# Kernel tuning notes

Hardware: AMD Instinct MI355X
Metric: run time of the kernel (lower is better)

The kernel has to match this reference:

```python
import jax, jax.numpy as jnp
import numpy as np

B, F, S = 2, 512, 1024
E = 4
I = 1024          # intermediate = 2 * features
K = 3             # conv kernel size
INIT_SCALE = 1.0
EPS = 1e-5
SLOPE = 0.02


def setup_inputs() -> dict:
    key = jax.random.key(0)
    k = jax.random.split(key, 6)
    inp = jax.random.normal(k[0], (B, F, S), jnp.float32)
    divisor = (jnp.arange(S, dtype=jnp.float32) + 1.0).reshape(1, 1, S)
    w0_gate = jax.random.normal(k[1], (E, F, 1), jnp.float32) * (F ** -0.5)
    w0 = jax.random.normal(k[2], (E, F, 3 * I), jnp.float32) * (F ** -0.5)
    w1 = jax.random.normal(k[3], (3 * I, I, K), jnp.float32) * ((I * K) ** -0.5)
    w2_gate = jax.random.normal(k[4], (E, I, 1), jnp.float32) * (I ** -0.5)
    w2 = jax.random.normal(k[5], (E, I, F), jnp.float32) * (I ** -0.5)
    return {"inp": inp, "divisor": divisor, "w0_gate": w0_gate, "w0": w0,
            "w1": w1, "w2_gate": w2_gate, "w2": w2}


def _norm(x):
    # channel norm over dim 1: subtract mean, divide by scaled L2 norm
    x = x - jnp.mean(x, axis=1, keepdims=True)
    n = jnp.sqrt(jnp.sum(x * x, axis=1, keepdims=True)) * (x.shape[1] ** -0.5)
    return x / (n + EPS)


def _moe(x, gate, w):
    # x: [B,F,S]; gate: [E,F,1]; w: [E,F,D]
    logits = jnp.einsum('bfs,ef->bes', x, gate[:, :, 0])          # [B,E,S]
    gates = jax.nn.softmax(logits, axis=1)
    idx = jnp.argmax(logits, axis=1)                              # [B,S]
    one_hot = jax.nn.one_hot(idx, w.shape[0], dtype=x.dtype)      # [B,S,E]
    # straight-through gumbel-style gate: hard one-hot fwd, soft grad
    gumbel = jnp.transpose(one_hot, (0, 2, 1)) - jax.lax.stop_gradient(gates) + gates  # [B,E,S]
    xs = jnp.transpose(x, (0, 2, 1))                              # [B,S,F]
    out = jnp.zeros((x.shape[0], x.shape[2], w.shape[2]), x.dtype)
    for e in range(w.shape[0]):  # small fixed expert count
        mask = one_hot[:, :, e][:, :, None]                       # [B,S,1]
        out = out + mask * ((xs * gumbel[:, e, :, None]) @ w[e])
    loss = jnp.sum(jnp.mean(gates, axis=(0, 2)) * jnp.mean(one_hot, axis=(0, 1)))
    return loss, jnp.transpose(out, (0, 2, 1))                    # [B,D,S]


def _conv1d(x, w, causal_pad):
    if causal_pad and w.shape[-1] > 1:
        x = jnp.pad(x, ((0, 0), (0, 0), (w.shape[-1] - 1, 0)))
    return jax.lax.conv_general_dilated(
        x, w, window_strides=(1,), padding='VALID',
        dimension_numbers=('NCH', 'OIH', 'NCH'), feature_group_count=1)


def reference(inp, divisor, w0_gate, w0, w1, w2_gate, w2):
    loss0, h = _moe(inp, w0_gate, w0)                 # [B,3I,S]
    depth, scale, shift = jnp.split(h, 3, axis=1)     # each [B,I,S]
    cum = jnp.cumsum(depth, axis=-1)
    h = jax.nn.leaky_relu(_norm(cum / divisor * scale + shift), SLOPE)
    h = _conv1d(h, w1, causal_pad=True)               # [B,3I,S]
    s0, s1, sh = jnp.split(h, 3, axis=1)
    h = jax.nn.leaky_relu(_norm(s0 * s1 + sh), SLOPE)
    loss1, out = _moe(h, w2_gate, w2)                 # [B,F,S]
    return out * INIT_SCALE, loss0 + loss1
```

## Files before the change

### kernel.cpp

```cpp
#include <hip/hip_runtime.h>
#include <hip/hip_bf16.h>

#define SDIM 1024

typedef float f32x4 __attribute__((ext_vector_type(4)));
typedef short short8 __attribute__((ext_vector_type(8)));

__device__ __forceinline__ unsigned short f2bf(float f) {
    __hip_bfloat16 h = __float2bfloat16(f);
    return *reinterpret_cast<unsigned short*>(&h);
}
__device__ __forceinline__ float bf2f(unsigned short u) {
    return __uint_as_float(((unsigned int)u) << 16);
}
__device__ __forceinline__ void gload_lds16(const unsigned short* g, unsigned short* l) {
    __builtin_amdgcn_global_load_lds((const __attribute__((address_space(1))) void*)g,
                                     (__attribute__((address_space(3))) void*)l, 16, 0, 0);
}

__device__ __forceinline__ void tr_split(
    const float* __restrict__ in, unsigned short* __restrict__ oh,
    unsigned short* __restrict__ ol, int R, int C, size_t sliceStride,
    int bx, int by, int slice, int tid, float (*t)[33])
{
    int c0 = bx * 32, r0 = by * 32;
    int cc = tid & 31, r8 = tid >> 5;
    const float* ip = in + slice * sliceStride;
    #pragma unroll
    for (int k = 0; k < 4; ++k) {
        int r = r8 + k * 8;
        t[r][cc] = ip[(size_t)(r0 + r) * C + c0 + cc];
    }
    __syncthreads();
    #pragma unroll
    for (int k = 0; k < 4; ++k) {
        int rr = r8 + k * 8;
        float v = t[cc][rr];
        unsigned short hi = f2bf(v);
        unsigned short lo = f2bf(v - bf2f(hi));
        size_t o = slice * sliceStride + (size_t)(c0 + rr) * R + r0 + cc;
        oh[o] = hi; ol[o] = lo;
    }
}

__global__ __launch_bounds__(256) void prep_kernel(
    const float* __restrict__ inp, const float* __restrict__ w0,
    const float* __restrict__ w1,
    unsigned short* __restrict__ xTh, unsigned short* __restrict__ xTl,
    unsigned short* __restrict__ w0Th, unsigned short* __restrict__ w0Tl,
    unsigned short* __restrict__ w1Th, unsigned short* __restrict__ w1Tl,
    const float* __restrict__ wg, int* __restrict__ idx, float* __restrict__ acc)
{
    __shared__ float t[32][33];
    __shared__ float wgs[4 * 512];
    __shared__ float part[32][4][9];
    __shared__ float la[8];
    int id = blockIdx.x;
    int tid = threadIdx.x;
    if (id < 1024) {
        int bx = id & 31, by = (id >> 5) & 15, slice = id >> 9;
        tr_split(inp, xTh, xTl, 512, 1024, (size_t)512 * 1024, bx, by, slice, tid, t);
    } else if (id < 7168) {
        int m = id - 1024;
        int bx = m % 96, by = (m / 96) & 15, slice = m / 1536;
        tr_split(w0, w0Th, w0Tl, 512, 3072, (size_t)512 * 3072, bx, by, slice, tid, t);
    } else if (id < 19456) {
        int tt = (id - 7168) * 256 + tid;
        int o = tt >> 10, i = tt & 1023;
        const float* p = w1 + (size_t)o * 3072 + i * 3;
        #pragma unroll
        for (int k = 0; k < 3; ++k) {
            float v = p[k];
            unsigned short hi = f2bf(v);
            unsigned short lo = f2bf(v - bf2f(hi));
            size_t off = (size_t)k * 3145728 + (size_t)o * 1024 + i;
            w1Th[off] = hi; w1Tl[off] = lo;
        }
    } else {
        if (tid < 8) la[tid] = 0.f;
        for (int l = tid; l < 2048; l += 256) wgs[l] = wg[l];
        __syncthreads();
        int t0 = (id - 19456) * 8;
        int b = t0 >> 10, s0 = t0 & 1023;
        int sl = tid & 7, fg = tid >> 3;
        float l0 = 0.f, l1 = 0.f, l2 = 0.f, l3 = 0.f;
        for (int f = fg; f < 512; f += 32) {
            float xv = inp[((size_t)b * 512 + f) * SDIM + s0 + sl];
            l0 += xv * wgs[f];
            l1 += xv * wgs[512 + f];
            l2 += xv * wgs[1024 + f];
            l3 += xv * wgs[1536 + f];
        }
        part[fg][0][sl] = l0; part[fg][1][sl] = l1;
        part[fg][2][sl] = l2; part[fg][3][sl] = l3;
        __syncthreads();
        for (int h = 16; h >= 1; h >>= 1) {
            if (fg < h) {
                #pragma unroll
                for (int e = 0; e < 4; ++e) part[fg][e][sl] += part[fg + h][e][sl];
            }
            __syncthreads();
        }
        if (fg == 0) {
            float L[4] = {part[0][0][sl], part[0][1][sl], part[0][2][sl], part[0][3][sl]};
            float m = fmaxf(fmaxf(L[0], L[1]), fmaxf(L[2], L[3]));
            float e0 = expf(L[0] - m), e1 = expf(L[1] - m), e2 = expf(L[2] - m), e3 = expf(L[3] - m);
            float inv = 1.0f / (e0 + e1 + e2 + e3);
            int best = 0; float bv = L[0];
            if (L[1] > bv) { bv = L[1]; best = 1; }
            if (L[2] > bv) { bv = L[2]; best = 2; }
            if (L[3] > bv) { bv = L[3]; best = 3; }
            idx[t0 + sl] = best;
            atomicAdd(&la[0], e0 * inv);
            atomicAdd(&la[1], e1 * inv);
            atomicAdd(&la[2], e2 * inv);
            atomicAdd(&la[3], e3 * inv);
            atomicAdd(&la[4 + best], 1.0f);
        }
        __syncthreads();
        if (tid < 8) atomicAdd(&acc[tid], la[tid]);
    }
}

__global__ __launch_bounds__(1024) void sort_kernel(
    const int* __restrict__ idx, int* __restrict__ perm, int* __restrict__ eSorted)
{
    int b = blockIdx.x;
    int tid = threadIdx.x;
    int lane = tid & 63, w = tid >> 6;
    int e = idx[(b << 10) + tid];
    __shared__ int wcnt[16][4];
    __shared__ int woff[16][4];
    int r = 0;
    unsigned long long lt = (1ull << lane) - 1ull;
    #pragma unroll
    for (int eo = 0; eo < 4; ++eo) {
        unsigned long long m = __ballot(e == eo);
        if (lane == 0) wcnt[w][eo] = __popcll(m);
        if (e == eo) r = __popcll(m & lt);
    }
    __syncthreads();
    if (tid == 0) {
        int baseAcc = 0;
        for (int eo = 0; eo < 4; ++eo)
            for (int ww = 0; ww < 16; ++ww) { woff[ww][eo] = baseAcc; baseAcc += wcnt[ww][eo]; }
    }
    __syncthreads();
    int pos = woff[w][e] + r;
    perm[(b << 10) + pos] = tid;
    eSorted[(b << 10) + pos] = e;
}

__global__ __launch_bounds__(256) void moe_split_kernel(
    const unsigned short* __restrict__ base, unsigned int XH, unsigned int XL,
    unsigned int WH, unsigned int WL,
    const int* __restrict__ perm, const int* __restrict__ eSorted,
    float* __restrict__ out, int Fdim, int Ddim)
{
    __shared__ unsigned short lds[768 * 32];
    int id = blockIdx.x;
    int chunk = gridDim.x >> 3;
    int wg = (id & 7) * chunk + (id >> 3);
    int t0 = (wg & 15) * 128;
    int d0 = (wg >> 4) * 64;
    int b = t0 >> 10, s0 = t0 & 1023;
    int tid = threadIdx.x;
    int lane = tid & 63;
    int lm = lane & 15, q = lane >> 4;
    int wid = tid >> 6;
    int wm = (wid >> 1) * 32, wn = (wid & 1) * 64;

    int eLo = eSorted[(b << 10) + s0];
    int eHi = eSorted[(b << 10) + s0 + 127];

    unsigned int gofs[12];
    int lofs[12], doSeg[12];
    #pragma unroll
    for (int j = 0; j < 12; ++j) {
        int seg = wid + 4 * j;
        int row = seg * 16 + (lane >> 2);
        int slot = lane & 3;
        int c = slot ^ ((row >> 1) & 3);
        unsigned int src;
        int act = 1;
        if (row < 256) {
            int gr = (row < 128) ? row : row - 128;
            unsigned int hb = (row < 128) ? XH : XL;
            int tj = perm[(b << 10) + s0 + gr];
            src = hb + (unsigned int)(((b << 10) + tj) * Fdim) + c * 8;
        } else {
            int R = row - 256;
            unsigned int hb = WH;
            if (R >= 256) { R -= 256; hb = WL; }
            int e = R >> 6;
            act = (e >= eLo && e <= eHi) ? 1 : 0;
            src = hb + (unsigned int)((e * Ddim + d0 + (R & 63)) * Fdim) + c * 8;
        }
        gofs[j] = src; lofs[j] = seg * 512 + lane * 8; doSeg[j] = act;
    }

    int bofH[4];
    #pragma unroll
    for (int fn = 0; fn < 4; ++fn) {
        int rh = wn + fn * 16 + lm;
        bofH[fn] = rh * 32 + ((q ^ ((rh >> 1) & 3)) << 3);
    }
    int aofH[4][2], aofL[4][2];
    #pragma unroll
    for (int e = 0; e < 4; ++e)
        #pragma unroll
        for (int fm = 0; fm < 2; ++fm) {
            int rh = 256 + e * 64 + wm + fm * 16 + lm;
            int rl = rh + 256;
            aofH[e][fm] = rh * 32 + ((q ^ ((rh >> 1) & 3)) << 3);
            aofL[e][fm] = rl * 32 + ((q ^ ((rl >> 1) & 3)) << 3);
        }

    int eidx[4], sv[4];
    #pragma unroll
    for (int fn = 0; fn < 4; ++fn) {
        int sl = (b << 10) + s0 + wn + fn * 16 + lm;
        eidx[fn] = eSorted[sl];
        sv[fn]   = perm[sl];
    }
    bool presF[4][4], presE[4];
    #pragma unroll
    for (int e = 0; e < 4; ++e) {
        presE[e] = false;
        #pragma unroll
        for (int fn = 0; fn < 4; ++fn) {
            presF[e][fn] = __any(eidx[fn] == e);
            presE[e] = presE[e] || presF[e][fn];
        }
    }

    f32x4 acc[2][4];
    #pragma unroll
    for (int fm = 0; fm < 2; ++fm)
        #pragma unroll
        for (int fn = 0; fn < 4; ++fn)
            acc[fm][fn] = (f32x4){0.f, 0.f, 0.f, 0.f};

    const short8 z = {0, 0, 0, 0, 0, 0, 0, 0};

    for (int f0 = 0; f0 < Fdim; f0 += 32) {
        __syncthreads();
        #pragma unroll
        for (int j = 0; j < 12; ++j)
            if (doSeg[j]) gload_lds16(base + gofs[j] + f0, lds + lofs[j]);
        __syncthreads();

        short8 bh[4], bl[4];
        #pragma unroll
        for (int fn = 0; fn < 4; ++fn) {
            bh[fn] = *(const short8*)(lds + bofH[fn]);
            bl[fn] = *(const short8*)(lds + bofH[fn] + 4096);
        }
        #pragma unroll
        for (int e = 0; e < 4; ++e) {
            if (presE[e]) {
                short8 ah[2], al[2];
                #pragma unroll
                for (int fm = 0; fm < 2; ++fm) {
                    ah[fm] = *(const short8*)(lds + aofH[e][fm]);
                    al[fm] = *(const short8*)(lds + aofL[e][fm]);
                }
                #pragma unroll
                for (int fn = 0; fn < 4; ++fn) {
                    if (presF[e][fn]) {
                        short8 bmH = (eidx[fn] == e) ? bh[fn] : z;
                        short8 bmL = (eidx[fn] == e) ? bl[fn] : z;
                        #pragma unroll
                        for (int fm = 0; fm < 2; ++fm) {
                            acc[fm][fn] = __builtin_amdgcn_mfma_f32_16x16x32_bf16(ah[fm], bmH, acc[fm][fn], 0, 0, 0);
                            acc[fm][fn] = __builtin_amdgcn_mfma_f32_16x16x32_bf16(ah[fm], bmL, acc[fm][fn], 0, 0, 0);
                            acc[fm][fn] = __builtin_amdgcn_mfma_f32_16x16x32_bf16(al[fm], bmH, acc[fm][fn], 0, 0, 0);
                        }
                    }
                }
            }
        }
    }

    #pragma unroll
    for (int fm = 0; fm < 2; ++fm)
        #pragma unroll
        for (int fn = 0; fn < 4; ++fn) {
            int d = d0 + wm + fm * 16 + q * 4;
            float* op = out + ((size_t)b * Ddim + d) * SDIM + sv[fn];
            #pragma unroll
            for (int r = 0; r < 4; ++r)
                op[(size_t)r * SDIM] = acc[fm][fn][r];
        }
}

__global__ __launch_bounds__(768) void conv_split_kernel(
    const unsigned short* __restrict__ base, unsigned int GH, unsigned int GL,
    unsigned int WH, unsigned int WL, unsigned int ZB, float* __restrict__ co)
{
    extern __shared__ unsigned short lds[];
    const int BUF = 35328;
    int id = blockIdx.x;
    int wg = (id & 7) * 32 + (id >> 3);
    int t0 = (wg & 7) * 256;
    int o0 = (wg >> 3) * 96;
    int b = t0 >> 10, s0 = t0 & 1023;
    int tid = threadIdx.x;
    int lane = tid & 63;
    int lm = lane & 15, q = lane >> 4;
    int wid = tid >> 6;
    int wm = (wid >> 2) * 32, wn = (wid & 3) * 64;

    unsigned int gofs[6];
    int lofs[6];
    int nseg = (wid < 9) ? 6 : 5;
    #pragma unroll
    for (int j = 0; j < 6; ++j) {
        int seg = wid + 12 * j;
        gofs[j] = ZB; lofs[j] = 0;
        if (seg < 69) {
            int row = seg * 16 + (lane >> 2);
            int slot = lane & 3;
            int c = slot ^ ((row >> 1) & 3);
            unsigned int src;
            if (row < 528) {
                int gr = (row < 264) ? row : row - 264;
                unsigned int hb = (row < 264) ? GH : GL;
                int s = s0 - 2 + gr;
                if (s < 0) src = ZB + c * 8;
                else { if (s > 1023) s = 1023;
                       src = hb + ((unsigned int)((b << 10) + s) << 10) + c * 8; }
            } else {
                int R = row - 528;
                unsigned int hb = WH;
                if (R >= 288) { R -= 288; hb = WL; }
                int k = R / 96, ol = R - k * 96;
                src = hb + (unsigned int)k * 3145728u + ((unsigned int)(o0 + ol) << 10) + c * 8;
            }
            gofs[j] = src;
            lofs[j] = seg * 512 + lane * 8;
        }
    }

    int aofH[3][2], aofL[3][2], bofH[3][4], bofL[3][4];
    #pragma unroll
    for (int k = 0; k < 3; ++k) {
        #pragma unroll
        for (int fm = 0; fm < 2; ++fm) {
            int R = k * 96 + wm + fm * 16 + lm;
            int rh = 528 + R, rl = 816 + R;
            aofH[k][fm] = rh * 32 + ((q ^ ((rh >> 1) & 3)) << 3);
            aofL[k][fm] = rl * 32 + ((q ^ ((rl >> 1) & 3)) << 3);
        }
        #pragma unroll
        for (int fn = 0; fn < 4; ++fn) {
            int rh = wn + fn * 16 + lm + k;
            int rl = rh + 264;
            bofH[k][fn] = rh * 32 + ((q ^ ((rh >> 1) & 3)) << 3);
            bofL[k][fn] = rl * 32 + ((q ^ ((rl >> 1) & 3)) << 3);
        }
    }

    f32x4 acc[2][4];
    #pragma unroll
    for (int fm = 0; fm < 2; ++fm)
        #pragma unroll
        for (int fn = 0; fn < 4; ++fn)
            acc[fm][fn] = (f32x4){0.f, 0.f, 0.f, 0.f};

    #pragma unroll
    for (int j = 0; j < 6; ++j)
        if (j < nseg) gload_lds16(base + gofs[j], lds + lofs[j]);

    int curOfs = 0;
    for (int i0 = 0; i0 < 1024; i0 += 32) {
        __syncthreads();
        int nxtOfs = curOfs ^ BUF;
        if (i0 + 32 < 1024) {
            #pragma unroll
            for (int j = 0; j < 6; ++j)
                if (j < nseg) gload_lds16(base + gofs[j] + i0 + 32, lds + nxtOfs + lofs[j]);
        }

        const unsigned short* lb = lds + curOfs;
        #pragma unroll
        for (int k = 0; k < 3; ++k) {
            short8 ah[2], al[2], bh[4], bl[4];
            #pragma unroll
            for (int fm = 0; fm < 2; ++fm) {
                ah[fm] = *(const short8*)(lb + aofH[k][fm]);
                al[fm] = *(const short8*)(lb + aofL[k][fm]);
            }
            #pragma unroll
            for (int fn = 0; fn < 4; ++fn) {
                bh[fn] = *(const short8*)(lb + bofH[k][fn]);
                bl[fn] = *(const short8*)(lb + bofL[k][fn]);
            }
            __builtin_amdgcn_s_setprio(1);
            #pragma unroll
            for (int fm = 0; fm < 2; ++fm)
                #pragma unroll
                for (int fn = 0; fn < 4; ++fn) {
                    acc[fm][fn] = __builtin_amdgcn_mfma_f32_16x16x32_bf16(ah[fm], bh[fn], acc[fm][fn], 0, 0, 0);
                    acc[fm][fn] = __builtin_amdgcn_mfma_f32_16x16x32_bf16(ah[fm], bl[fn], acc[fm][fn], 0, 0, 0);
                    acc[fm][fn] = __builtin_amdgcn_mfma_f32_16x16x32_bf16(al[fm], bh[fn], acc[fm][fn], 0, 0, 0);
                }
            __builtin_amdgcn_s_setprio(0);
        }
        curOfs = nxtOfs;
    }

    #pragma unroll
    for (int fm = 0; fm < 2; ++fm)
        #pragma unroll
        for (int fn = 0; fn < 4; ++fn) {
            int o = o0 + wm + fm * 16 + q * 4;
            int s = s0 + wn + fn * 16 + lm;
            float* op = co + ((size_t)b * 3072 + o) * SDIM + s;
            #pragma unroll
            for (int r = 0; r < 4; ++r)
                op[(size_t)r * SDIM] = acc[fm][fn][r];
        }
}

__global__ __launch_bounds__(256) void moe_kernel(
    const unsigned short* __restrict__ xT, const unsigned short* __restrict__ wT,
    const int* __restrict__ perm, const int* __restrict__ eSorted,
    float* __restrict__ out, int Fdim, int Ddim, const float* __restrict__ accv)
{
    if (blockIdx.x == 0 && threadIdx.x == 0) {
        float l = 0.f;
        #pragma unroll
        for (int e = 0; e < 4; ++e)
            l += accv[e] * accv[4 + e] + accv[8 + e] * accv[12 + e];
        out[2 * 512 * 1024] = l * (1.0f / (2048.0f * 2048.0f));
    }
    __shared__ unsigned short lds[384 * 32];
    int id = blockIdx.x;
    int chunk = gridDim.x >> 3;
    int wg = (id & 7) * chunk + (id >> 3);
    int t0 = (wg & 15) * 128;
    int d0 = (wg >> 4) * 64;
    int b = t0 >> 10, s0 = t0 & 1023;
    int tid = threadIdx.x;
    int lane = tid & 63, wid = tid >> 6;
    int lm = lane & 15, q = lane >> 4;
    int wm = (wid >> 1) * 32, wn = (wid & 1) * 64;

    int eLo = eSorted[(b << 10) + s0];
    int eHi = eSorted[(b << 10) + s0 + 127];

    const unsigned short* gsrc[6];
    int lofs[6], doSeg[6];
    #pragma unroll
    for (int j = 0; j < 6; ++j) {
        int seg = wid + 4 * j;
        int row = seg * 16 + (lane >> 2);
        int slot = lane & 3;
        int c = slot ^ ((row >> 1) & 3);
        int act = 1;
        const unsigned short* src;
        if (row < 128) {
            int tj = perm[(b << 10) + s0 + row];
            src = xT + (size_t)((b << 10) + tj) * Fdim + c * 8;
        } else {
            int R = row - 128;
            int e = R >> 6;
            act = (e >= eLo && e <= eHi) ? 1 : 0;
            src = wT + (size_t)(e * Ddim + d0 + (R & 63)) * Fdim + c * 8;
        }
        gsrc[j] = src; lofs[j] = seg * 512 + lane * 8; doSeg[j] = act;
    }

    int bof[4], aof[4][2];
    #pragma unroll
    for (int fn = 0; fn < 4; ++fn) {
        int row = wn + fn * 16 + lm;
        bof[fn] = row * 32 + ((q ^ ((row >> 1) & 3)) << 3);
    }
    #pragma unroll
    for (int e = 0; e < 4; ++e)
        #pragma unroll
        for (int fm = 0; fm < 2; ++fm) {
            int R = 128 + e * 64 + wm + fm * 16 + lm;
            aof[e][fm] = R * 32 + ((q ^ ((R >> 1) & 3)) << 3);
        }

    int eidx[4], sv[4];
    #pragma unroll
    for (int fn = 0; fn < 4; ++fn) {
        int sl = (b << 10) + s0 + wn + fn * 16 + lm;
        eidx[fn] = eSorted[sl];
        sv[fn]   = perm[sl];
    }
    bool presF[4][4], presE[4];
    #pragma unroll
    for (int e = 0; e < 4; ++e) {
        presE[e] = false;
        #pragma unroll
        for (int fn = 0; fn < 4; ++fn) {
            presF[e][fn] = __any(eidx[fn] == e);
            presE[e] = presE[e] || presF[e][fn];
        }
    }

    f32x4 acc[2][4];
    #pragma unroll
    for (int fm = 0; fm < 2; ++fm)
        #pragma unroll
        for (int fn = 0; fn < 4; ++fn)
            acc[fm][fn] = (f32x4){0.f, 0.f, 0.f, 0.f};

    const short8 z = {0, 0, 0, 0, 0, 0, 0, 0};

    for (int f0 = 0; f0 < Fdim; f0 += 32) {
        __syncthreads();
        #pragma unroll
        for (int j = 0; j < 6; ++j)
            if (doSeg[j]) gload_lds16(gsrc[j] + f0, lds + lofs[j]);
        __syncthreads();

        short8 bf[4];
        #pragma unroll
        for (int fn = 0; fn < 4; ++fn)
            bf[fn] = *(const short8*)(lds + bof[fn]);
        #pragma unroll
        for (int e = 0; e < 4; ++e) {
            if (presE[e]) {
                short8 af[2];
                #pragma unroll
                for (int fm = 0; fm < 2; ++fm)
                    af[fm] = *(const short8*)(lds + aof[e][fm]);
                #pragma unroll
                for (int fn = 0; fn < 4; ++fn) {
                    if (presF[e][fn]) {
                        short8 bm = (eidx[fn] == e) ? bf[fn] : z;
                        #pragma unroll
                        for (int fm = 0; fm < 2; ++fm)
                            acc[fm][fn] = __builtin_amdgcn_mfma_f32_16x16x32_bf16(af[fm], bm, acc[fm][fn], 0, 0, 0);
                    }
                }
            }
        }
    }

    #pragma unroll
    for (int fm = 0; fm < 2; ++fm)
        #pragma unroll
        for (int fn = 0; fn < 4; ++fn) {
            int d = d0 + wm + fm * 16 + q * 4;
            float* op = out + ((size_t)b * Ddim + d) * SDIM + sv[fn];
            #pragma unroll
            for (int r = 0; r < 4; ++r)
                op[(size_t)r * SDIM] = acc[fm][fn][r];
        }
}

__global__ __launch_bounds__(256) void cumsum_w2t_kernel(
    const float* __restrict__ h1, const float* __restrict__ divisor,
    float* __restrict__ y, const float* __restrict__ w2, unsigned short* __restrict__ w2T)
{
    __shared__ float tsh[32][33];
    __shared__ float wsum[4];
    int blk = blockIdx.x;
    int tid = threadIdx.x;
    if (blk >= 2048) {
        int m = blk - 2048;
        int bx = m & 15, by = (m >> 4) & 31, slice = m >> 9;
        int c0 = bx * 32, r0 = by * 32;
        int cc = tid & 31, r8 = tid >> 5;
        const float* ip = w2 + (size_t)slice * 524288;
        unsigned short* op = w2T + (size_t)slice * 524288;
        #pragma unroll
        for (int k = 0; k < 4; ++k) {
            int r = r8 + k * 8;
            tsh[r][cc] = ip[(size_t)(r0 + r) * 512 + c0 + cc];
        }
        __syncthreads();
        #pragma unroll
        for (int k = 0; k < 4; ++k) {
            int rr = r8 + k * 8;
            op[(size_t)(c0 + rr) * 1024 + r0 + cc] = f2bf(tsh[cc][rr]);
        }
        return;
    }
    int b = blk >> 10, i = blk & 1023;
    const float4* dp = (const float4*)(h1 + ((size_t)b * 3072 + i) * SDIM);
    const float4* sp = (const float4*)(h1 + ((size_t)b * 3072 + 1024 + i) * SDIM);
    const float4* hp = (const float4*)(h1 + ((size_t)b * 3072 + 2048 + i) * SDIM);
    float4 v = dp[tid];
    float c0 = v.x, c1 = c0 + v.y, c2 = c1 + v.z, c3 = c2 + v.w;
    int lane = tid & 63, w = tid >> 6;
    float sc = c3;
    #pragma unroll
    for (int off = 1; off < 64; off <<= 1) {
        float p = __shfl_up(sc, off);
        if (lane >= off) sc += p;
    }
    if (lane == 63) wsum[w] = sc;
    __syncthreads();
    float wbase = 0.f;
    #pragma unroll
    for (int ww = 0; ww < 4; ++ww)
        if (ww < w) wbase += wsum[ww];
    float base = wbase + sc - c3;
    float4 scv = sp[tid], sh = hp[tid];
    float4 dv = ((const float4*)divisor)[tid];
    float4 o;
    o.x = (base + c0) / dv.x * scv.x + sh.x;
    o.y = (base + c1) / dv.y * scv.y + sh.y;
    o.z = (base + c2) / dv.z * scv.z + sh.z;
    o.w = (base + c3) / dv.w * scv.w + sh.w;
    ((float4*)(y + ((size_t)b * 1024 + i) * SDIM))[tid] = o;
}

__global__ __launch_bounds__(256) void norm0_kernel(
    const float* __restrict__ g, unsigned short* __restrict__ oh,
    unsigned short* __restrict__ ol)
{
    int blk = blockIdx.x;
    int b = blk >> 7;
    int s0 = (blk & 127) * 8;
    int tid = threadIdx.x;
    int sg = tid & 7, grp = tid >> 3;
    int s = s0 + sg;
    const float* bp = g + ((size_t)b * 1024) * SDIM + s;
    float v[32];
    float sum = 0.f, ssq = 0.f;
    #pragma unroll
    for (int j = 0; j < 32; ++j) {
        float x = bp[(size_t)(grp * 32 + j) * SDIM];
        v[j] = x; sum += x; ssq += x * x;
    }
    __shared__ float rs[32][8], rq[32][8], stat[2][8];
    rs[grp][sg] = sum; rq[grp][sg] = ssq;
    __syncthreads();
    for (int h = 16; h >= 1; h >>= 1) {
        if (grp < h) { rs[grp][sg] += rs[grp + h][sg]; rq[grp][sg] += rq[grp + h][sg]; }
        __syncthreads();
    }
    if (grp == 0) {
        float S1 = rs[0][sg], S2 = rq[0][sg];
        float mean = S1 * (1.0f / 1024.0f);
        float ssc = fmaxf(S2 - 1024.0f * mean * mean, 0.0f);
        stat[0][sg] = mean;
        stat[1][sg] = 1.0f / (sqrtf(ssc) * (1.0f / 32.0f) + 1e-5f);
    }
    __syncthreads();
    float mean = stat[0][sg], inv = stat[1][sg];
    size_t tbase = (((size_t)b << 10) + s) * 1024 + grp * 32;
    #pragma unroll
    for (int j0 = 0; j0 < 32; j0 += 4) {
        unsigned short uh[4], ul[4];
        #pragma unroll
        for (int jj = 0; jj < 4; ++jj) {
            float o = (v[j0 + jj] - mean) * inv;
            o = (o >= 0.f) ? o : 0.02f * o;
            uh[jj] = f2bf(o);
            ul[jj] = f2bf(o - bf2f(uh[jj]));
        }
        *(ushort4*)(oh + tbase + j0) = (ushort4){uh[0], uh[1], uh[2], uh[3]};
        *(ushort4*)(ol + tbase + j0) = (ushort4){ul[0], ul[1], ul[2], ul[3]};
    }
}

__global__ __launch_bounds__(256) void normgate_kernel(
    const float* __restrict__ h1, const float* __restrict__ wg,
    unsigned short* __restrict__ outT, int* __restrict__ idx, float* __restrict__ acc)
{
    int blk = blockIdx.x;
    int b = blk >> 7;
    int s0 = (blk & 127) * 8;
    int tid = threadIdx.x;
    int sg = tid & 7, grp = tid >> 3;
    int s = s0 + sg;
    const float* bp = h1 + ((size_t)b * 3072) * SDIM + s;
    float v[32];
    float sum = 0.f, ssq = 0.f;
    #pragma unroll
    for (int j = 0; j < 32; ++j) {
        int i = grp * 32 + j;
        float a  = bp[(size_t)i * SDIM];
        float m2 = bp[(size_t)(1024 + i) * SDIM];
        float d2 = bp[(size_t)(2048 + i) * SDIM];
        float x = a * m2 + d2;
        v[j] = x; sum += x; ssq += x * x;
    }
    __shared__ float rs[32][8], rq[32][8], stat[2][8];
    rs[grp][sg] = sum; rq[grp][sg] = ssq;
    __syncthreads();
    for (int h = 16; h >= 1; h >>= 1) {
        if (grp < h) { rs[grp][sg] += rs[grp + h][sg]; rq[grp][sg] += rq[grp + h][sg]; }
        __syncthreads();
    }
    if (grp == 0) {
        float S1 = rs[0][sg], S2 = rq[0][sg];
        float mean = S1 * (1.0f / 1024.0f);
        float ssc = fmaxf(S2 - 1024.0f * mean * mean, 0.0f);
        stat[0][sg] = mean;
        stat[1][sg] = 1.0f / (sqrtf(ssc) * (1.0f / 32.0f) + 1e-5f);
    }
    __syncthreads();
    float mean = stat[0][sg], inv = stat[1][sg];
    float l0 = 0.f, l1 = 0.f, l2 = 0.f, l3 = 0.f;
    size_t tbase = (((size_t)b << 10) + s) * 1024 + grp * 32;
    #pragma unroll
    for (int j0 = 0; j0 < 32; j0 += 4) {
        unsigned short u[4];
        #pragma unroll
        for (int jj = 0; jj < 4; ++jj) {
            int i = grp * 32 + j0 + jj;
            float o = (v[j0 + jj] - mean) * inv;
            o = (o >= 0.f) ? o : 0.02f * o;
            u[jj] = f2bf(o);
            l0 += o * wg[i];
            l1 += o * wg[1024 + i];
            l2 += o * wg[2048 + i];
            l3 += o * wg[3072 + i];
        }
        *(ushort4*)(outT + tbase + j0) = (ushort4){u[0], u[1], u[2], u[3]};
    }
    __shared__ float pl[4][32][8];
    __shared__ float la[8];
    pl[0][grp][sg] = l0; pl[1][grp][sg] = l1;
    pl[2][grp][sg] = l2; pl[3][grp][sg] = l3;
    if (tid < 8) la[tid] = 0.f;
    __syncthreads();
    for (int h = 16; h >= 1; h >>= 1) {
        if (grp < h) {
            #pragma unroll
            for (int e = 0; e < 4; ++e) pl[e][grp][sg] += pl[e][grp + h][sg];
        }
        __syncthreads();
    }
    if (grp == 0) {
        float L[4] = {pl[0][0][sg], pl[1][0][sg], pl[2][0][sg], pl[3][0][sg]};
        float m = fmaxf(fmaxf(L[0], L[1]), fmaxf(L[2], L[3]));
        float e0 = expf(L[0] - m), e1 = expf(L[1] - m), e2 = expf(L[2] - m), e3 = expf(L[3] - m);
        float invs = 1.0f / (e0 + e1 + e2 + e3);
        int best = 0; float bv = L[0];
        if (L[1] > bv) { bv = L[1]; best = 1; }
        if (L[2] > bv) { bv = L[2]; best = 2; }
        if (L[3] > bv) { bv = L[3]; best = 3; }
        idx[(b << 10) + s] = best;
        atomicAdd(&la[0], e0 * invs);
        atomicAdd(&la[1], e1 * invs);
        atomicAdd(&la[2], e2 * invs);
        atomicAdd(&la[3], e3 * invs);
        atomicAdd(&la[4 + best], 1.0f);
    }
    __syncthreads();
    if (tid < 8) atomicAdd(&acc[8 + tid], la[tid]);
}

extern "C" void kernel_launch(void* const* d_in, const int* in_sizes, int n_in,
                              void* d_out, int out_size, void* d_ws, size_t ws_size,
                              hipStream_t stream) {
    const float* inp     = (const float*)d_in[0];
    const float* divisor = (const float*)d_in[1];
    const float* w0_gate = (const float*)d_in[2];
    const float* w0      = (const float*)d_in[3];
    const float* w1      = (const float*)d_in[4];
    const float* w2_gate = (const float*)d_in[5];
    const float* w2      = (const float*)d_in[6];
    float* out = (float*)d_out;
    (void)in_sizes; (void)n_in; (void)out_size; (void)ws_size;

    char* ws = (char*)d_ws;
    const unsigned short* base = (const unsigned short*)ws;

    float* h1            = (float*)(ws + 0);
    float* g             = (float*)(ws + 25165824);
    unsigned short* gT1h = (unsigned short*)(ws + 33554432);
    unsigned short* gT1l = (unsigned short*)(ws + 37748736);
    unsigned short* w1Th = (unsigned short*)(ws + 41943040);
    unsigned short* w1Tl = (unsigned short*)(ws + 60817408);
    unsigned short* xTh  = (unsigned short*)(ws + 79691776);
    unsigned short* xTl  = (unsigned short*)(ws + 81788928);
    unsigned short* w0Th = (unsigned short*)(ws + 83886080);
    unsigned short* w0Tl = (unsigned short*)(ws + 96468992);
    unsigned short* gT2  = (unsigned short*)(ws + 79691776);
    unsigned short* w2T  = (unsigned short*)(ws + 83886080);
    int* idx1            = (int*)(ws + 109051904);
    int* idx2            = (int*)(ws + 109060096);
    float* acc           = (float*)(ws + 109068288);
    int* perm1           = (int*)(ws + 109076480);
    int* eSort1          = (int*)(ws + 109084672);
    int* perm2           = (int*)(ws + 109092864);
    int* eSort2          = (int*)(ws + 109101056);
    float* zbuf          = (float*)(ws + 109109248);

    const unsigned int GT1H = 16777216u, GT1L = 18874368u;
    const unsigned int W1TH = 20971520u, W1TL = 30408704u;
    const unsigned int XTH  = 39845888u, XTL  = 40894464u;
    const unsigned int W0TH = 41943040u, W0TL = 48234496u;
    const unsigned int ZB   = 54554624u;

    hipMemsetAsync(acc, 0, 64, stream);
    hipMemsetAsync(zbuf, 0, 4096, stream);

    prep_kernel<<<19712, 256, 0, stream>>>(inp, w0, w1, xTh, xTl, w0Th, w0Tl,
                                           w1Th, w1Tl, w0_gate, idx1, acc);

    sort_kernel<<<2, 1024, 0, stream>>>(idx1, perm1, eSort1);
    moe_split_kernel<<<768, 256, 0, stream>>>(base, XTH, XTL, W0TH, W0TL, perm1, eSort1, h1, 512, 3072);

    cumsum_w2t_kernel<<<4096, 256, 0, stream>>>(h1, divisor, g, w2, w2T);
    norm0_kernel<<<256, 256, 0, stream>>>(g, gT1h, gT1l);
    conv_split_kernel<<<256, 768, 141312, stream>>>(base, GT1H, GT1L, W1TH, W1TL, ZB, h1);
    normgate_kernel<<<256, 256, 0, stream>>>(h1, w2_gate, gT2, idx2, acc);

    sort_kernel<<<2, 1024, 0, stream>>>(idx2, perm2, eSort2);
    moe_kernel<<<128, 256, 0, stream>>>(gT2, w2T, perm2, eSort2, out, 1024, 512, acc);
}
```

Baseline: 244.9 us.

## Retile first MoE GEMM to larger 768-thread blocks with double-buffered LDS prefetch

The first split-bf16 MoE GEMM now uses 256 blocks of 768 threads, each covering 256 tokens by 96 output rows, in place of 768 blocks of 256 threads covering 128 by 64. Global-to-LDS loads for the next K slice are issued into a second 80 KB buffer while MFMAs run on the current one, so there is one barrier per step and no separate wait for loads. The wave scheduling priority is raised around the MFMA block. The cost is 160 KB of dynamic LDS per block, which allows only one block per CU, and far fewer blocks in total.

```diff
diff --git a/kernel.cpp b/kernel.cpp
--- a/kernel.cpp
+++ b/kernel.cpp
@@ -151,69 +151,72 @@
     eSorted[(b << 10) + pos] = e;
 }
 
-__global__ __launch_bounds__(256) void moe_split_kernel(
+__global__ __launch_bounds__(768) void moe_split_kernel(
     const unsigned short* __restrict__ base, unsigned int XH, unsigned int XL,
     unsigned int WH, unsigned int WL,
     const int* __restrict__ perm, const int* __restrict__ eSorted,
-    float* __restrict__ out, int Fdim, int Ddim)
+    float* __restrict__ out)
 {
-    __shared__ unsigned short lds[768 * 32];
+    extern __shared__ unsigned short lds[];
+    const int BUF = 40960;
     int id = blockIdx.x;
-    int chunk = gridDim.x >> 3;
-    int wg = (id & 7) * chunk + (id >> 3);
-    int t0 = (wg & 15) * 128;
-    int d0 = (wg >> 4) * 64;
+    int wg = (id & 7) * 32 + (id >> 3);
+    int t0 = (wg & 7) * 256;
+    int d0 = (wg >> 3) * 96;
     int b = t0 >> 10, s0 = t0 & 1023;
     int tid = threadIdx.x;
     int lane = tid & 63;
     int lm = lane & 15, q = lane >> 4;
     int wid = tid >> 6;
-    int wm = (wid >> 1) * 32, wn = (wid & 1) * 64;
+    int wm = (wid >> 2) * 32, wn = (wid & 3) * 64;
 
     int eLo = eSorted[(b << 10) + s0];
-    int eHi = eSorted[(b << 10) + s0 + 127];
-
-    unsigned int gofs[12];
-    int lofs[12], doSeg[12];
-    #pragma unroll
-    for (int j = 0; j < 12; ++j) {
-        int seg = wid + 4 * j;
-        int row = seg * 16 + (lane >> 2);
-        int slot = lane & 3;
-        int c = slot ^ ((row >> 1) & 3);
-        unsigned int src;
-        int act = 1;
-        if (row < 256) {
-            int gr = (row < 128) ? row : row - 128;
-            unsigned int hb = (row < 128) ? XH : XL;
-            int tj = perm[(b << 10) + s0 + gr];
-            src = hb + (unsigned int)(((b << 10) + tj) * Fdim) + c * 8;
-        } else {
-            int R = row - 256;
-            unsigned int hb = WH;
-            if (R >= 256) { R -= 256; hb = WL; }
-            int e = R >> 6;
-            act = (e >= eLo && e <= eHi) ? 1 : 0;
-            src = hb + (unsigned int)((e * Ddim + d0 + (R & 63)) * Fdim) + c * 8;
-        }
-        gofs[j] = src; lofs[j] = seg * 512 + lane * 8; doSeg[j] = act;
+    int eHi = eSorted[(b << 10) + s0 + 255];
+
+    unsigned int gofs[7];
+    int lofs[7], doSeg[7];
+    #pragma unroll
+    for (int j = 0; j < 7; ++j) {
+        int seg = wid + 12 * j;
+        gofs[j] = 0; lofs[j] = 0; doSeg[j] = 0;
+        if (seg < 80) {
+            int row = seg * 16 + (lane >> 2);
+            int slot = lane & 3;
+            int c = slot ^ ((row >> 1) & 3);
+            unsigned int src;
+            int act = 1;
+            if (row < 512) {
+                int gr = (row < 256) ? row : row - 256;
+                unsigned int hb = (row < 256) ? XH : XL;
+                int tj = perm[(b << 10) + s0 + gr];
+                src = hb + (unsigned int)(((b << 10) + tj) * 512) + c * 8;
+            } else {
+                int R = row - 512;
+                unsigned int hb = WH;
+                if (R >= 384) { R -= 384; hb = WL; }
+                int e = R / 96, dl = R - e * 96;
+                act = (e >= eLo && e <= eHi) ? 1 : 0;
+                src = hb + (unsigned int)((e * 3072 + d0 + dl) * 512) + c * 8;
+            }
+            gofs[j] = src;
+            lofs[j] = seg * 512 + lane * 8;
+            doSeg[j] = act;
+        }
     }
 
     int bofH[4];
     #pragma unroll
     for (int fn = 0; fn < 4; ++fn) {
-        int rh = wn + fn * 16 + lm;
-        bofH[fn] = rh * 32 + ((q ^ ((rh >> 1) & 3)) << 3);
-    }
-    int aofH[4][2], aofL[4][2];
+        int row = wn + fn * 16 + lm;
+        bofH[fn] = row * 32 + ((q ^ ((row >> 1) & 3)) << 3);
+    }
+    int aofH[4][2];
     #pragma unroll
     for (int e = 0; e < 4; ++e)
         #pragma unroll
         for (int fm = 0; fm < 2; ++fm) {
-            int rh = 256 + e * 64 + wm + fm * 16 + lm;
-            int rl = rh + 256;
-            aofH[e][fm] = rh * 32 + ((q ^ ((rh >> 1) & 3)) << 3);
-            aofL[e][fm] = rl * 32 + ((q ^ ((rl >> 1) & 3)) << 3);
+            int row = 512 + e * 96 + wm + fm * 16 + lm;
+            aofH[e][fm] = row * 32 + ((q ^ ((row >> 1) & 3)) << 3);
         }
 
     int eidx[4], sv[4];
@@ -243,18 +246,26 @@
 
     const short8 z = {0, 0, 0, 0, 0, 0, 0, 0};
 
-    for (int f0 = 0; f0 < Fdim; f0 += 32) {
-        __syncthreads();
-        #pragma unroll
-        for (int j = 0; j < 12; ++j)
-            if (doSeg[j]) gload_lds16(base + gofs[j] + f0, lds + lofs[j]);
-        __syncthreads();
-
+    #pragma unroll
+    for (int j = 0; j < 7; ++j)
+        if (doSeg[j]) gload_lds16(base + gofs[j], lds + lofs[j]);
+
+    int curOfs = 0;
+    for (int f0 = 0; f0 < 512; f0 += 32) {
+        __syncthreads();
+        int nxtOfs = curOfs ^ BUF;
+        if (f0 + 32 < 512) {
+            #pragma unroll
+            for (int j = 0; j < 7; ++j)
+                if (doSeg[j]) gload_lds16(base + gofs[j] + f0 + 32, lds + nxtOfs + lofs[j]);
+        }
+
+        const unsigned short* lb = lds + curOfs;
         short8 bh[4], bl[4];
         #pragma unroll
         for (int fn = 0; fn < 4; ++fn) {
-            bh[fn] = *(const short8*)(lds + bofH[fn]);
-            bl[fn] = *(const short8*)(lds + bofH[fn] + 4096);
+            bh[fn] = *(const short8*)(lb + bofH[fn]);
+            bl[fn] = *(const short8*)(lb + bofH[fn] + 8192);
         }
         #pragma unroll
         for (int e = 0; e < 4; ++e) {
@@ -262,9 +273,10 @@
                 short8 ah[2], al[2];
                 #pragma unroll
                 for (int fm = 0; fm < 2; ++fm) {
-                    ah[fm] = *(const short8*)(lds + aofH[e][fm]);
-                    al[fm] = *(const short8*)(lds + aofL[e][fm]);
+                    ah[fm] = *(const short8*)(lb + aofH[e][fm]);
+                    al[fm] = *(const short8*)(lb + aofH[e][fm] + 12288);
                 }
+                __builtin_amdgcn_s_setprio(1);
                 #pragma unroll
                 for (int fn = 0; fn < 4; ++fn) {
                     if (presF[e][fn]) {
@@ -278,8 +290,10 @@
                         }
                     }
                 }
+                __builtin_amdgcn_s_setprio(0);
             }
         }
+        curOfs = nxtOfs;
     }
 
     #pragma unroll
@@ -287,7 +301,7 @@
         #pragma unroll
         for (int fn = 0; fn < 4; ++fn) {
             int d = d0 + wm + fm * 16 + q * 4;
-            float* op = out + ((size_t)b * Ddim + d) * SDIM + sv[fn];
+            float* op = out + ((size_t)b * 3072 + d) * SDIM + sv[fn];
             #pragma unroll
             for (int r = 0; r < 4; ++r)
                 op[(size_t)r * SDIM] = acc[fm][fn][r];
@@ -803,7 +817,7 @@
                                            w1Th, w1Tl, w0_gate, idx1, acc);
 
     sort_kernel<<<2, 1024, 0, stream>>>(idx1, perm1, eSort1);
-    moe_split_kernel<<<768, 256, 0, stream>>>(base, XTH, XTL, W0TH, W0TL, perm1, eSort1, h1, 512, 3072);
+    moe_split_kernel<<<256, 768, 163840, stream>>>(base, XTH, XTL, W0TH, W0TL, perm1, eSort1, h1);
 
     cumsum_w2t_kernel<<<4096, 256, 0, stream>>>(h1, divisor, g, w2, w2T);
     norm0_kernel<<<256, 256, 0, stream>>>(g, gT1h, gT1l);
```

Result: faster. 239.3 us (-2.3%).
